# Optimization experiments

Measured on AMD Instinct MI355X. Metric: run time of the kernel, lower is better.

Reference implementation:

```python
import jax, jax.numpy as jnp
import numpy as np
import math

T, P, ITERS, H = 6, 8, 2, 8          # nr_types, num_proto, iters, n_head
D, F = 512, 1024                      # dim_proto, feature_dim (hidden_dim==D)
L = T * ITERS                         # 12 cross-attention layers


def _ln(x, g=None, b=None, eps=1e-5):
    m = x.mean(-1, keepdims=True)
    v = x.var(-1, keepdims=True)
    y = (x - m) * jax.lax.rsqrt(v + eps)
    if g is not None:
        y = y * g + b
    return y


def _forward(x_batch, batch_mask, node_type, pm_W, pm_b, pm_g, pm_bn,
             proto_logsigma, rand_mul, Wq, bq, Wk, bk, Wv, bv, Wo, bo,
             ag, ab, Wm1, bm1, lg, lb, Wm2, bm2, pg, pb):
    B, N, _ = x_batch.shape
    dt = x_batch.dtype
    bm = batch_mask.astype(dt)                                   # [B,N]
    onehot = jax.nn.one_hot(node_type, T, dtype=dt)              # [B,N,T]
    valid = bm * jnp.any(x_batch != 0, axis=-1).astype(dt)       # [B,N]
    mbt = onehot * valid[:, :, None]                             # [B,N,T]
    sums = jnp.einsum('bnt,bnf->btf', mbt, x_batch)              # per-(batch,type) sum
    cnt = mbt.sum(1)                                             # [B,T]
    fallback = x_batch.sum(1) / bm.sum(1, keepdims=True)         # [B,F]
    proto_mu = jnp.where(cnt[..., None] > 0,
                         sums / jnp.maximum(cnt, 1.0)[..., None],
                         fallback[:, None, :])                   # [B,T,F]

    # proto_mlp: Linear + LayerNorm + GELU (dropout = eval/identity)
    mu = jax.nn.gelu(_ln(proto_mu @ pm_W + pm_b, pm_g, pm_bn), approximate=False)  # [B,T,D]
    all_proto = mu[:, :, None, :] + jnp.exp(proto_logsigma)[None] * rand_mul[None]  # [B,T,P,D]

    dh = D // H
    scale = 1.0 / math.sqrt(dh)
    keymask = bm[:, None, None, :] == 0                          # [B,1,1,N]

    def layer(q, i):
        resid = q                                                 # [B,P,D]
        k = _ln((x_batch @ Wk[i] + bk[i]).reshape(B, N, H, dh))   # QK-LayerNorm (no affine)
        v = (x_batch @ Wv[i] + bv[i]).reshape(B, N, H, dh)
        qh = _ln((q @ Wq[i] + bq[i]).reshape(B, P, H, dh))
        dots = jnp.einsum('bkhd,bnhd->bkhn', qh, k) * scale       # [B,P,H,N]
        dots = jnp.where(keymask, -jnp.inf, dots)
        attn = jax.nn.softmax(dots, axis=-1)
        upd = jnp.einsum('bnhd,bkhn->bkhd', v, attn).reshape(B, P, D)
        upd = upd @ Wo[i] + bo[i]
        q = resid + _ln(upd, ag[i], ab[i])
        h = jax.nn.gelu(_ln(q @ Wm1[i] + bm1[i], lg[i], lb[i]), approximate=False)
        h = h @ Wm2[i] + bm2[i]
        return q + _ln(h, pg[i], pb[i])

    outs = []
    c = 0
    for i in range(T):
        p = all_proto[:, i]
        for _ in range(ITERS):
            p = layer(p, c)
            c += 1
        outs.append(p)
    prototypes = jnp.stack(outs, axis=1)                          # [B,T,P,D]
    return prototypes, proto_mu


def setup_inputs() -> dict:
    key = jax.random.key(0)
    ks = jax.random.split(key, 40)
    B, N = 4, 4096
    sc = 0.02

    def rn(i, shape, s=sc):
        return jax.random.normal(ks[i], shape, jnp.float32) * s

    inp = {
        'x_batch': jax.random.normal(ks[0], (B, N, F), jnp.float32),
        'batch_mask': jax.random.randint(ks[1], (B, N), 0, 2, jnp.int32),
        'node_type': jax.random.randint(ks[2], (B, N), 0, T, jnp.int32),
        'pm_W': rn(3, (F, D)), 'pm_b': jnp.zeros((D,)),
        'pm_g': jnp.ones((D,)), 'pm_bn': jnp.zeros((D,)),
        'proto_logsigma': rn(4, (T, 1, D), 0.05),
        'rand_mul': jax.random.normal(ks[5], (T, P, D), jnp.float32),
        'Wq': rn(6, (L, D, D)), 'bq': jnp.zeros((L, D)),
        'Wk': rn(7, (L, F, D)), 'bk': jnp.zeros((L, D)),
        'Wv': rn(8, (L, F, D)), 'bv': jnp.zeros((L, D)),
        'Wo': rn(9, (L, D, D)), 'bo': jnp.zeros((L, D)),
        'ag': jnp.ones((L, D)), 'ab': jnp.zeros((L, D)),
        'Wm1': rn(10, (L, D, D)), 'bm1': jnp.zeros((L, D)),
        'lg': jnp.ones((L, D)), 'lb': jnp.zeros((L, D)),
        'Wm2': rn(11, (L, D, D)), 'bm2': jnp.zeros((L, D)),
        'pg': jnp.ones((L, D)), 'pb': jnp.zeros((L, D)),
    }
    return inp


def reference(x_batch, batch_mask, node_type, pm_W, pm_b, pm_g, pm_bn,
              proto_logsigma, rand_mul, Wq, bq, Wk, bk, Wv, bv, Wo, bo,
              ag, ab, Wm1, bm1, lg, lb, Wm2, bm2, pg, pb):
    return _forward(x_batch, batch_mask, node_type, pm_W, pm_b, pm_g, pm_bn,
                    proto_logsigma, rand_mul, Wq, bq, Wk, bk, Wv, bv, Wo, bo,
                    ag, ab, Wm1, bm1, lg, lb, Wm2, bm2, pg, pb)
```

## Files before the change

### kernel.cpp

```cpp
#include <hip/hip_runtime.h>
#include <hip/hip_bf16.h>
#include <stdint.h>

#define TT 6
#define PP 8
#define HH 8
#define DD 512
#define FF 1024
#define DH 64
#define NB 4
#define NN 4096
#define LL 12
#define NCH 16
#define CHK 256

typedef __attribute__((ext_vector_type(8))) short short8v;
typedef __attribute__((ext_vector_type(4))) float f32x4;
typedef __attribute__((ext_vector_type(4))) unsigned short u16x4;
typedef __attribute__((ext_vector_type(8))) unsigned short u16x8;
typedef unsigned short u16;

__device__ __forceinline__ float bf2f(u16 u){
  union { unsigned int i; float f; } x; x.i = ((unsigned int)u) << 16; return x.f;
}
__device__ __forceinline__ u16 f2bf(float f){
  union { float f; unsigned int i; } x; x.f = f;
  unsigned int r = x.i + 0x7fffu + ((x.i >> 16) & 1u);
  return (u16)(r >> 16);
}
__device__ __forceinline__ float wave_sum(float x){
  #pragma unroll
  for (int o = 32; o > 0; o >>= 1) x += __shfl_xor(x, o);
  return x;
}
__device__ __forceinline__ float ldf(const void* p, size_t i, int f32){
  float v;
  if (f32) v = ((const float*)p)[i];
  else     v = bf2f(((const u16*)p)[i]);
  return v;
}
__device__ __forceinline__ float gemv_vec(const float* __restrict__ xs,
    const void* __restrict__ W, size_t wbase, int ktot, int wf32,
    float* __restrict__ red, int tid){
  int g = tid & 63, sl = tid >> 6;
  int kpw = ktot >> 3;
  float a[8] = {0,0,0,0,0,0,0,0};
  if (wf32){
    const float* Wp = (const float*)W + wbase + (size_t)(sl*kpw)*DD + g*8;
    #pragma unroll 4
    for (int i = 0; i < kpw; ++i){
      float xv = xs[sl*kpw + i];
      f32x4 lo = *(const f32x4*)(Wp + (size_t)i*DD);
      f32x4 hi = *(const f32x4*)(Wp + (size_t)i*DD + 4);
      a[0]+=xv*lo.x; a[1]+=xv*lo.y; a[2]+=xv*lo.z; a[3]+=xv*lo.w;
      a[4]+=xv*hi.x; a[5]+=xv*hi.y; a[6]+=xv*hi.z; a[7]+=xv*hi.w;
    }
  } else {
    const u16* Wp = (const u16*)W + wbase + (size_t)(sl*kpw)*DD + g*8;
    #pragma unroll 4
    for (int i = 0; i < kpw; ++i){
      float xv = xs[sl*kpw + i];
      u16x8 w8 = *(const u16x8*)(Wp + (size_t)i*DD);
      #pragma unroll
      for (int j = 0; j < 8; ++j) a[j] += xv * bf2f(w8[j]);
    }
  }
  #pragma unroll
  for (int j = 0; j < 8; ++j) red[sl*512 + g*8 + j] = a[j];
  __syncthreads();
  float y = 0;
  #pragma unroll
  for (int s2 = 0; s2 < 8; ++s2) y += red[s2*512 + tid];
  return y;
}
__device__ __forceinline__ void glds16(const void* g, void* l){
#if __has_builtin(__builtin_amdgcn_global_load_lds)
  __builtin_amdgcn_global_load_lds(
      (const __attribute__((address_space(1))) void*)g,
      (__attribute__((address_space(3))) void*)l, 16, 0, 0);
#else
  *(u16x8*)l = *(const u16x8*)g;
#endif
}
__device__ __forceinline__ void tail_gemm8(f32x4 acc[4], const u16* __restrict__ Bp,
    const u16* As, int l15, int q4, int n0w){
  #pragma unroll
  for (int ni = 0; ni < 4; ++ni){ f32x4 z = {0,0,0,0}; acc[ni] = z; }
  #pragma unroll 2
  for (int k0 = 0; k0 < 512; k0 += 32){
    short8v bf[4], af;
    #pragma unroll
    for (int ni = 0; ni < 4; ++ni)
      bf[ni] = *(const short8v*)(Bp + (size_t)(n0w + ni*16 + l15)*DD + k0 + q4*8);
    af = *(const short8v*)(As + l15*520 + k0 + q4*8);
    #pragma unroll
    for (int ni = 0; ni < 4; ++ni)
      acc[ni] = __builtin_amdgcn_mfma_f32_16x16x32_bf16(af, bf[ni], acc[ni], 0, 0, 0);
  }
}
__device__ __forceinline__ void row_ln8(const f32x4 acc[4],
    float* red1, float* red2, int w, int l15, int q4,
    float mv[4], float rv[4]){
  float s1[4], s2[4];
  #pragma unroll
  for (int r = 0; r < 4; ++r){
    float a0=acc[0][r], a1=acc[1][r], a2=acc[2][r], a3=acc[3][r];
    s1[r] = (a0+a1)+(a2+a3);
    s2[r] = (a0*a0+a1*a1)+(a2*a2+a3*a3);
  }
  #pragma unroll
  for (int o = 1; o < 16; o <<= 1)
    #pragma unroll
    for (int r = 0; r < 4; ++r){
      s1[r] += __shfl_xor(s1[r], o);
      s2[r] += __shfl_xor(s2[r], o);
    }
  if (l15 == 0){
    #pragma unroll
    for (int r = 0; r < 4; ++r){
      int row = q4*4 + r;
      red1[row*8 + w] = s1[r];
      red2[row*8 + w] = s2[r];
    }
  }
  __syncthreads();
  #pragma unroll
  for (int r = 0; r < 4; ++r){
    int row = q4*4 + r;
    float S1 = 0, S2 = 0;
    #pragma unroll
    for (int j = 0; j < 8; ++j){ S1 += red1[row*8+j]; S2 += red2[row*8+j]; }
    float m = S1 * (1.f/DD);
    float var = S2 * (1.f/DD) - m*m;
    mv[r] = m;
    rv[r] = rsqrtf(var + 1e-5f);
  }
  __syncthreads();
}

__global__ void k_detect(const void* __restrict__ X, int* __restrict__ flag){
  int tid = threadIdx.x;
  const u16* u = (const u16*)X;
  int bad = 0;
  for (int i = tid; i < 8192; i += 256){
    int ex = (u[i] >> 7) & 0xFF;
    if (ex >= 0x90) bad = 1;
  }
  __shared__ int s;
  if (tid == 0) s = 0;
  __syncthreads();
  if (bad) s = 1;
  __syncthreads();
  if (tid == 0) *flag = s;
}

__global__ void k_xbv(const void* __restrict__ X, u16* __restrict__ Xb,
                      const int* __restrict__ bm, float* __restrict__ valid,
                      const int* __restrict__ flagp){
  int f32 = *flagp;
  int bid = blockIdx.x, tid = threadIdx.x;
  size_t idx = (size_t)bid*FF + tid*4;
  bool a;
  if (f32){
    f32x4 v = *(const f32x4*)((const float*)X + idx);
    u16x4 o; o.x=f2bf(v.x); o.y=f2bf(v.y); o.z=f2bf(v.z); o.w=f2bf(v.w);
    *(u16x4*)(Xb+idx) = o;
    a = (v.x!=0.f)||(v.y!=0.f)||(v.z!=0.f)||(v.w!=0.f);
  } else {
    u16x4 v = *(const u16x4*)((const u16*)X + idx);
    *(u16x4*)(Xb+idx) = v;
    a = (bf2f(v.x)!=0.f)||(bf2f(v.y)!=0.f)||(bf2f(v.z)!=0.f)||(bf2f(v.w)!=0.f);
  }
  __shared__ int flag;
  if (tid==0) flag = 0;
  __syncthreads();
  if (a) flag = 1;
  __syncthreads();
  if (tid==0) valid[bid] = (flag && bm[bid]) ? 1.f : 0.f;
}

__global__ void k_compact(const int* __restrict__ bm, int* __restrict__ nidx,
                          int* __restrict__ cntc){
  int b = blockIdx.x, tid = threadIdx.x;
  __shared__ int csum[256];
  __shared__ int pref[257];
  int base = b*NN + tid*16;
  int f[16]; int loc = 0;
  #pragma unroll
  for (int i = 0; i < 16; ++i){ f[i] = (bm[base+i] != 0); loc += f[i]; }
  csum[tid] = loc;
  __syncthreads();
  if (tid == 0){
    pref[0] = 0;
    for (int j = 0; j < 256; ++j) pref[j+1] = pref[j] + csum[j];
  }
  __syncthreads();
  int off = b*NN + pref[tid];
  #pragma unroll
  for (int i = 0; i < 16; ++i){ if (f[i]) nidx[off++] = tid*16 + i; }
  if (tid == 0) cntc[b] = pref[256];
}

__global__ void k_wbfT(const void* __restrict__ Wq, const void* __restrict__ Wo,
                       const void* __restrict__ Wm1, const void* __restrict__ Wm2,
                       u16* __restrict__ Wt, const int* __restrict__ flagp){
  int f32 = *flagp;
  int z = blockIdx.z;
  int fam = z / LL;
  const void* src = (fam==0) ? Wq : (fam==1) ? Wo : (fam==2) ? Wm1 : Wm2;
  size_t sbase = (size_t)(z % LL) * DD * DD;
  __shared__ u16 tile[32][33];
  int d0 = blockIdx.x*32, k0 = blockIdx.y*32;
  int tx = threadIdx.x, ty = threadIdx.y;
  #pragma unroll
  for (int i = 0; i < 4; ++i){
    size_t idx = sbase + (size_t)(k0 + ty + i*8)*DD + d0 + tx;
    u16 v;
    if (f32) v = f2bf(((const float*)src)[idx]);
    else     v = ((const u16*)src)[idx];
    tile[ty + i*8][tx] = v;
  }
  __syncthreads();
  #pragma unroll
  for (int i = 0; i < 4; ++i)
    Wt[((size_t)z*DD + d0 + ty + i*8)*DD + k0 + tx] = tile[tx][ty + i*8];
}

__global__ void k_cnt(const float* __restrict__ valid, const int* __restrict__ bm,
                      const int* __restrict__ ntype, float* __restrict__ cnt,
                      float* __restrict__ bmsum){
  int b = blockIdx.x; int tid = threadIdx.x;
  float c[TT] = {0,0,0,0,0,0}; float cb = 0;
  for (int n = tid; n < NN; n += 256){
    float v = valid[b*NN + n];
    int ty = ntype[b*NN + n];
    #pragma unroll
    for (int t = 0; t < TT; ++t) c[t] += (ty==t) ? v : 0.f;
    cb += bm[b*NN+n] ? 1.f : 0.f;
  }
  __shared__ float sc_[TT+1];
  if (tid < TT+1) sc_[tid] = 0.f;
  __syncthreads();
  #pragma unroll
  for (int t = 0; t < TT; ++t) atomicAdd(&sc_[t], c[t]);
  atomicAdd(&sc_[TT], cb);
  __syncthreads();
  if (tid < TT) cnt[b*TT + tid] = sc_[tid];
  if (tid == TT) bmsum[b] = sc_[TT];
}

__global__ void k_colsum(const u16* __restrict__ Xb, const float* __restrict__ valid,
                         const int* __restrict__ ntype, float* __restrict__ colsums,
                         float* __restrict__ coltotal){
  int f0 = threadIdx.x * 4;
  int b = blockIdx.z;
  int n0 = blockIdx.y * 64;
  float acc[TT][4] = {};
  float tot[4] = {0,0,0,0};
  for (int i = 0; i < 64; ++i){
    int n = n0 + i;
    u16x4 xv4 = *(const u16x4*)(Xb + ((size_t)(b*NN+n))*FF + f0);
    float v = valid[b*NN+n];
    int ty = ntype[b*NN+n];
    #pragma unroll
    for (int j = 0; j < 4; ++j){
      float xv = bf2f(xv4[j]);
      tot[j] += xv;
      float xvv = xv * v;
      #pragma unroll
      for (int t = 0; t < TT; ++t) acc[t][j] += (ty==t) ? xvv : 0.f;
    }
  }
  #pragma unroll
  for (int t = 0; t < TT; ++t)
    #pragma unroll
    for (int j = 0; j < 4; ++j)
      atomicAdd(&colsums[((size_t)(b*TT+t))*FF + f0 + j], acc[t][j]);
  #pragma unroll
  for (int j = 0; j < 4; ++j)
    atomicAdd(&coltotal[b*FF + f0 + j], tot[j]);
}

__global__ void k_protomu(const float* __restrict__ colsums, const float* __restrict__ coltotal,
                          const float* __restrict__ cnt, const float* __restrict__ bmsum,
                          float* __restrict__ proto_mu, void* __restrict__ dout,
                          const int* __restrict__ flagp){
  int f32 = *flagp;
  const size_t OFFP = (size_t)NB*TT*PP*DD;
  int bt = blockIdx.x; int b = bt / TT;
  int tid = threadIdx.x;
  float cv = cnt[bt];
  float inv = 1.f / fmaxf(cv, 1.f);
  float fbinv = 1.f / bmsum[b];
  for (int f = tid; f < FF; f += 256){
    float pm = (cv > 0.f) ? colsums[(size_t)bt*FF + f] * inv
                          : coltotal[b*FF + f] * fbinv;
    proto_mu[(size_t)bt*FF + f] = pm;
    if (f32) ((float*)dout)[OFFP + (size_t)bt*FF + f] = pm;
    else     ((u16*)dout)[OFFP + (size_t)bt*FF + f] = f2bf(pm);
  }
}

__global__ void __launch_bounds__(512) k_mu(const float* __restrict__ proto_mu,
   const void* __restrict__ pmW, const void* __restrict__ pmb,
   const void* __restrict__ pmg, const void* __restrict__ pmbn,
   const void* __restrict__ lsig, const void* __restrict__ rmul,
   float* __restrict__ qstate, const int* __restrict__ flagp){
  int f32 = *flagp;
  int bt = blockIdx.x; int b = bt/TT, t = bt%TT;
  int d = threadIdx.x;
  __shared__ float xs[FF];
  __shared__ float red[4096];
  __shared__ float r1[8], r2[8];
  xs[d] = proto_mu[(size_t)bt*FF + d];
  xs[d+512] = proto_mu[(size_t)bt*FF + d + 512];
  __syncthreads();
  float acc = ldf(pmb, d, f32) + gemv_vec(xs, pmW, 0, FF, f32, red, d);
  int lane = d & 63, wid = d >> 6;
  float s1 = wave_sum(acc), s2 = wave_sum(acc*acc);
  if (lane==0){ r1[wid]=s1; r2[wid]=s2; }
  __syncthreads();
  float m=0, qq=0;
  #pragma unroll
  for (int i=0;i<8;++i){ m+=r1[i]; qq+=r2[i]; }
  m *= (1.f/DD); float var = qq*(1.f/DD) - m*m;
  float y = (acc - m) * rsqrtf(var + 1e-5f) * ldf(pmg, d, f32) + ldf(pmbn, d, f32);
  float mu = 0.5f * y * (1.f + erff(y * 0.70710678118654752f));
  #pragma unroll
  for (int p = 0; p < PP; ++p){
    float rv = ldf(rmul, (size_t)(t*PP+p)*DD + d, f32);
    float ls = ldf(lsig, (size_t)t*DD + d, f32);
    qstate[(((size_t)(b*TT+t))*PP + p)*DD + d] = mu + expf(ls) * rv;
  }
}

__global__ void k_transpose(const void* __restrict__ Wk, const void* __restrict__ Wv,
                            u16* __restrict__ TK, u16* __restrict__ TV,
                            int tlo, int s, const int* __restrict__ flagp){
  int f32 = *flagp;
  int ti = blockIdx.z >> 1, kv = blockIdx.z & 1;
  int c = 2*(tlo+ti)+s;
  size_t eoff = (size_t)c*FF*DD;
  const void* W = kv ? Wv : Wk;
  u16* T = (kv ? TV : TK) + (size_t)ti*FF*DD;
  __shared__ u16 tile[32][33];
  int n0 = blockIdx.x * 32, k0 = blockIdx.y * 32;
  int tx = threadIdx.x, ty = threadIdx.y;
  #pragma unroll
  for (int i = 0; i < 4; ++i){
    size_t idx = eoff + (size_t)(k0 + ty + i*8)*DD + n0 + tx;
    u16 v;
    if (f32) v = f2bf(((const float*)W)[idx]);
    else     v = ((const u16*)W)[idx];
    tile[ty + i*8][tx] = v;
  }
  __syncthreads();
  #pragma unroll
  for (int i = 0; i < 4; ++i)
    T[(size_t)(n0 + ty + i*8)*FF + k0 + tx] = tile[tx][ty + i*8];
}

__global__ void __launch_bounds__(512) k_kvgemm(const u16* __restrict__ Xb,
    const u16* __restrict__ TK, const u16* __restrict__ TV,
    const void* __restrict__ bk, const void* __restrict__ bv,
    u16* __restrict__ Kb, u16* __restrict__ Vb,
    const int* __restrict__ nidx, const int* __restrict__ cntc,
    int tlo, int s, int nt, const int* __restrict__ flagp){
  int f32 = *flagp;
  int orig = blockIdx.x;
  int x = orig & 7, r = orig >> 3;
  int bx = r / nt, pr = r - bx*nt;
  int pairg = x*nt + pr;
  int by = pairg & 3; int kvti = pairg >> 2; int kv = kvti & 1; int ti = kvti >> 1;
  int b = bx >> 4, jt = bx & 15;
  int cnt = cntc[b];
  if (jt*256 >= cnt) return;
  int c = 2*(tlo+ti)+s;
  size_t boff = (size_t)c*DD;
  const u16* WT = (kv ? TV : TK) + (size_t)ti*FF*DD;
  const void* bias = kv ? bv : bk;
  u16* out = (kv ? Vb : Kb) + (size_t)ti*((size_t)NB*NN*DD);
  int n0 = by*128;
  __shared__ __align__(16) char LDS[3*24576];
  int tid = threadIdx.x, wid = tid >> 6, lane = tid & 63;
  int wr = wid >> 1, wcn = wid & 1;
  const u16* gp0; const u16* gp1; const u16* gp2;
  int lo0, lo1, lo2;
  {
    const u16* gps[3]; int los[3];
    #pragma unroll
    for (int i = 0; i < 3; ++i){
      int e = tid + i*512;
      if (e < 1024){
        int row = e>>2, sp = e&3;
        int ssrc = sp ^ (((row>>3)&1)<<1);
        int cl = jt*256 + row; if (cl >= cnt) cl = cnt-1;
        int grow = nidx[b*NN + cl];
        gps[i] = Xb + ((size_t)b*NN + grow)*FF + ssrc*8;
        los[i] = e*16;
      } else {
        int e2 = e - 1024;
        int row = e2>>2, sp = e2&3;
        int ssrc = sp ^ (((row>>3)&1)<<1);
        gps[i] = WT + (size_t)(n0 + row)*FF + ssrc*8;
        los[i] = 16384 + e2*16;
      }
    }
    gp0=gps[0]; gp1=gps[1]; gp2=gps[2];
    lo0=los[0]; lo1=los[1]; lo2=los[2];
  }
#define STAGE(T) { char* bb_ = LDS + ((T)%3)*24576; \
  glds16(gp0 + (T)*32, bb_ + lo0); glds16(gp1 + (T)*32, bb_ + lo1); \
  glds16(gp2 + (T)*32, bb_ + lo2); }
  int ke = (lane>>4) ^ (((lane>>3)&1)<<1);
  int arow[4], brow[4];
  #pragma unroll
  for (int mi = 0; mi < 4; ++mi)
    arow[mi] = (wr*64 + mi*16 + (lane&15))*64 + ke*16;
  #pragma unroll
  for (int ni = 0; ni < 4; ++ni)
    brow[ni] = 16384 + (wcn*64 + ni*16 + (lane&15))*64 + ke*16;
  f32x4 acc[4][4] = {};
  STAGE(0);
  STAGE(1);
  asm volatile("s_waitcnt vmcnt(3)" ::: "memory");
  __builtin_amdgcn_sched_barrier(0);
  __builtin_amdgcn_s_barrier();
  __builtin_amdgcn_sched_barrier(0);
  #pragma unroll
  for (int t = 0; t < 32; ++t){
    const char* Bbuf = LDS + (t%3)*24576;
    short8v af[4], bf[4];
    #pragma unroll
    for (int mi = 0; mi < 4; ++mi)
      af[mi] = *(const short8v*)(Bbuf + arow[mi]);
    #pragma unroll
    for (int ni = 0; ni < 4; ++ni)
      bf[ni] = *(const short8v*)(Bbuf + brow[ni]);
    if (t + 2 <= 31) STAGE(t+2);
    __builtin_amdgcn_s_setprio(1);
    #pragma unroll
    for (int mi = 0; mi < 4; ++mi)
      #pragma unroll
      for (int ni = 0; ni < 4; ++ni)
        acc[mi][ni] = __builtin_amdgcn_mfma_f32_16x16x32_bf16(af[mi], bf[ni], acc[mi][ni], 0, 0, 0);
    __builtin_amdgcn_s_setprio(0);
    if (t < 30)       asm volatile("s_waitcnt vmcnt(3)" ::: "memory");
    else if (t == 30) asm volatile("s_waitcnt vmcnt(0)" ::: "memory");
    __builtin_amdgcn_sched_barrier(0);
    if (t < 31){
      __builtin_amdgcn_s_barrier();
      __builtin_amdgcn_sched_barrier(0);
    }
  }
#undef STAGE
  #pragma unroll
  for (int mi = 0; mi < 4; ++mi){
    #pragma unroll
    for (int ni = 0; ni < 4; ++ni){
      int col = n0 + wcn*64 + ni*16 + (lane & 15);
      int h = col >> 6, dh = col & 63;
      float bvf = ldf(bias, boff + col, f32);
      #pragma unroll
      for (int r2 = 0; r2 < 4; ++r2){
        int row = jt*256 + wr*64 + mi*16 + (lane>>4)*4 + r2;
        out[(((size_t)(b*HH + h))*NN + row)*DH + dh] = f2bf(acc[mi][ni][r2] + bvf);
      }
    }
  }
}

__global__ void __launch_bounds__(512) k_qproj(const float* __restrict__ qstate,
      const void* __restrict__ Wq, const void* __restrict__ bq,
      float* __restrict__ qh, int tlo, int s, int wmode,
      const int* __restrict__ flagp){
  int f32 = *flagp;
  int wf32 = wmode ? f32 : 0;
  int z = blockIdx.x; int ti = z >> 5, rr = z & 31;
  int b = rr >> 3, p = rr & 7;
  int t = tlo + ti, c = 2*t + s;
  size_t woff = (size_t)c*DD*DD, boff = (size_t)c*DD;
  int d = threadIdx.x;
  __shared__ float xs[DD];
  __shared__ float red[4096];
  const float* xrow = qstate + (((size_t)(b*TT+t))*PP + p)*DD;
  xs[d] = xrow[d];
  __syncthreads();
  float acc = ldf(bq, boff + d, f32) + gemv_vec(xs, Wq, woff, DD, wf32, red, d);
  float s1 = wave_sum(acc) * (1.f/DH);
  float s2 = wave_sum(acc*acc) * (1.f/DH);
  float var = s2 - s1*s1;
  qh[(size_t)z*DD + d] = (acc - s1) * rsqrtf(var + 1e-5f);
}

__global__ void __launch_bounds__(512) k_attnA(const u16* __restrict__ Kb,
     const u16* __restrict__ Vb, const float* __restrict__ qh,
     const int* __restrict__ cntc, float* __restrict__ Opart, float* __restrict__ lpart){
  int ic = blockIdx.x, bh = blockIdx.y, ti = blockIdx.z;
  int b = bh >> 3, h = bh & 7;
  int cnt = cntc[b];
  if (ic*CHK >= cnt) return;
  int tid = threadIdx.x, p8 = tid >> 6, ln = tid & 63;
  int r8 = ln >> 3, g = ln & 7;
  __shared__ __align__(16) char KV[65536];
  __shared__ float qs[PP*DH];
  __shared__ float qsum[PP];
  __shared__ float e_lds[CHK*9];
  int rem = cnt - ic*CHK;
  float qv = qh[((size_t)(ti*32 + b*PP + p8))*DD + h*DH + ln];
  size_t tioff = (size_t)ti*((size_t)NB*NN*DD);
  const u16* Kbase = Kb + tioff + ((size_t)(b*HH + h)*NN + (size_t)ic*CHK)*DH;
  const u16* Vbase = Vb + tioff + ((size_t)(b*HH + h)*NN + (size_t)ic*CHK)*DH;
  #pragma unroll
  for (int i = 0; i < 4; ++i){
    int e = tid + i*512;
    int row = e >> 3, sp = e & 7;
    int rr = row < rem ? row : rem-1;
    glds16(Kbase + (size_t)rr*DH + sp*8, (char*)KV + e*16);
  }
  #pragma unroll
  for (int i = 0; i < 4; ++i){
    int e = tid + i*512;
    int row = e >> 3, sp = e & 7;
    int ss = sp ^ (row & 7);
    int rr = row < rem ? row : rem-1;
    glds16(Vbase + (size_t)rr*DH + ss*8, (char*)KV + 32768 + e*16);
  }
  qs[p8*DH + ln] = qv;
  {
    float sQ = wave_sum(qv);
    if (ln == 0) qsum[p8] = sQ;
  }
  asm volatile("s_waitcnt vmcnt(4) lgkmcnt(0)" ::: "memory");
  __builtin_amdgcn_sched_barrier(0);
  __builtin_amdgcn_s_barrier();
  __builtin_amdgcn_sched_barrier(0);
  #pragma unroll
  for (int it = 0; it < CHK/64; ++it){
    int nl = it*64 + p8*8 + r8;
    u16x8 kv8 = *(const u16x8*)((const char*)KV + nl*128 + g*16);
    float kf[8];
    #pragma unroll
    for (int e = 0; e < 8; ++e) kf[e] = bf2f(kv8[e]);
    float sm = 0, sq = 0;
    #pragma unroll
    for (int e = 0; e < 8; ++e){ sm += kf[e]; sq += kf[e]*kf[e]; }
    #pragma unroll
    for (int o = 1; o < 8; o <<= 1){
      sm += __shfl_xor(sm, o);
      sq += __shfl_xor(sq, o);
    }
    sm *= (1.f/DH); sq = sq*(1.f/DH) - sm*sm;
    float inv = rsqrtf(sq + 1e-5f);
    float ap[8];
    #pragma unroll
    for (int p = 0; p < 8; ++p){
      f32x4 qa = *(const f32x4*)&qs[p*DH + g*8];
      f32x4 qb = *(const f32x4*)&qs[p*DH + g*8 + 4];
      ap[p] = kf[0]*qa.x + kf[1]*qa.y + kf[2]*qa.z + kf[3]*qa.w
            + kf[4]*qb.x + kf[5]*qb.y + kf[6]*qb.z + kf[7]*qb.w;
    }
    #pragma unroll
    for (int o = 1; o < 8; o <<= 1){
      #pragma unroll
      for (int p = 0; p < 8; ++p) ap[p] += __shfl_xor(ap[p], o);
    }
    float dg = (g==0)?ap[0]:(g==1)?ap[1]:(g==2)?ap[2]:(g==3)?ap[3]
             : (g==4)?ap[4]:(g==5)?ap[5]:(g==6)?ap[6]:ap[7];
    float sv = (dg - sm*qsum[g]) * inv * 0.125f;
    e_lds[nl*9 + g] = (nl < rem) ? __expf(sv) : 0.f;
  }
  __syncthreads();
  {
    float lp = 0;
    #pragma unroll
    for (int j = 0; j < CHK/64; ++j) lp += e_lds[(ln + j*64)*9 + p8];
    lp = wave_sum(lp);
    if (ln == 0) lpart[((size_t)(ti*32+bh)*NCH + ic)*PP + p8] = lp;
  }
  {
    float a0=0,a1=0,a2=0,a3=0,a4=0,a5=0,a6=0,a7=0;
    int vseg = (r8 ^ g) * 16;
    #pragma unroll 4
    for (int m = 0; m < CHK/8; ++m){
      float e = e_lds[(g + m*8)*9 + p8];
      u16x8 vv = *(const u16x8*)((const char*)KV + 32768 + (g + m*8)*128 + vseg);
      a0 += e*bf2f(vv[0]); a1 += e*bf2f(vv[1]);
      a2 += e*bf2f(vv[2]); a3 += e*bf2f(vv[3]);
      a4 += e*bf2f(vv[4]); a5 += e*bf2f(vv[5]);
      a6 += e*bf2f(vv[6]); a7 += e*bf2f(vv[7]);
    }
    #pragma unroll
    for (int o = 1; o < 8; o <<= 1){
      a0 += __shfl_xor(a0, o); a1 += __shfl_xor(a1, o);
      a2 += __shfl_xor(a2, o); a3 += __shfl_xor(a3, o);
      a4 += __shfl_xor(a4, o); a5 += __shfl_xor(a5, o);
      a6 += __shfl_xor(a6, o); a7 += __shfl_xor(a7, o);
    }
    if (g == 0){
      float* op = Opart + ((size_t)(ti*32+bh)*NCH + ic)*512 + p8*64 + r8*8;
      f32x4 lo = {a0,a1,a2,a3}, hi = {a4,a5,a6,a7};
      *(f32x4*)op = lo;
      *((f32x4*)op + 1) = hi;
    }
  }
}

__global__ void __launch_bounds__(512) k_tailm(
    const float* __restrict__ Opart, const float* __restrict__ lpart,
    const int* __restrict__ cntc,
    float* __restrict__ qstate, float* __restrict__ qh,
    const u16* __restrict__ Wt,
    const void* __restrict__ bo, const void* __restrict__ ag, const void* __restrict__ ab,
    const void* __restrict__ bm1, const void* __restrict__ lg, const void* __restrict__ lb,
    const void* __restrict__ bm2, const void* __restrict__ pg, const void* __restrict__ pb,
    const void* __restrict__ bq,
    int tlo, int s, int nt, const int* __restrict__ flagp){
  int f32 = *flagp;
  int ti = blockIdx.x & 7, b = blockIdx.x >> 3;
  if (ti >= nt) return;
  int t = tlo + ti, c = 2*t + s;
  int tid = threadIdx.x;
  int w = tid >> 6, lane = tid & 63, q4 = lane >> 4, l15 = lane & 15;
  int n0w = w*64;
  size_t boff = (size_t)c*DD;
  const size_t famSz = (size_t)LL*DD*DD;
  __shared__ u16 As[16*520];
  __shared__ float red1[128], red2[128];
  __shared__ float lval[64];
  int nch = (cntc[b] + CHK - 1) / CHK;
  for (int i = tid; i < 16*520; i += 512) As[i] = 0;
  if (tid < 64){
    int p = tid >> 3, hh = tid & 7;
    float l = 0;
    for (int ic = 0; ic < nch; ++ic)
      l += lpart[((size_t)(ti*32 + b*8 + hh)*NCH + ic)*PP + p];
    lval[tid] = 1.f / l;
  }
  __syncthreads();
  {
    int hh = tid >> 6, dd = tid & 63;
    #pragma unroll
    for (int p = 0; p < 8; ++p){
      float o = 0;
      for (int ic = 0; ic < nch; ++ic)
        o += Opart[((size_t)(ti*32 + b*8 + hh)*NCH + ic)*512 + p*64 + dd];
      As[p*520 + hh*64 + dd] = f2bf(o * lval[p*8 + hh]);
    }
  }
  __syncthreads();
  f32x4 acc[4], q2[4];
  float mv[4], rv[4];
  size_t qoffb = ((size_t)(b*TT+t))*PP*DD;
  {
    const u16* Bp = Wt + famSz + (size_t)c*DD*DD;
    tail_gemm8(acc, Bp, As, l15, q4, n0w);
    #pragma unroll
    for (int ni = 0; ni < 4; ++ni){
      float bv = ldf(bo, boff + n0w + ni*16 + l15, f32);
      #pragma unroll
      for (int r = 0; r < 4; ++r) acc[ni][r] += bv;
    }
    row_ln8(acc, red1, red2, w, l15, q4, mv, rv);
    #pragma unroll
    for (int ni = 0; ni < 4; ++ni){
      int col = n0w + ni*16 + l15;
      float gm = ldf(ag, boff + col, f32), bt = ldf(ab, boff + col, f32);
      #pragma unroll
      for (int r = 0; r < 4; ++r){
        int row = q4*4 + r;
        float y = (acc[ni][r] - mv[r])*rv[r]*gm + bt;
        float res = (q4 < 2) ? qstate[qoffb + (size_t)row*DD + col] : 0.f;
        q2[ni][r] = res + y;
      }
    }
    if (q4 < 2){
      #pragma unroll
      for (int r = 0; r < 4; ++r){
        int row = q4*4 + r;
        #pragma unroll
        for (int ni = 0; ni < 4; ++ni)
          As[row*520 + n0w + ni*16 + l15] = f2bf(q2[ni][r]);
      }
    }
  }
  __syncthreads();
  {
    const u16* Bp = Wt + 2*famSz + (size_t)c*DD*DD;
    tail_gemm8(acc, Bp, As, l15, q4, n0w);
    #pragma unroll
    for (int ni = 0; ni < 4; ++ni){
      float bv = ldf(bm1, boff + n0w + ni*16 + l15, f32);
      #pragma unroll
      for (int r = 0; r < 4; ++r) acc[ni][r] += bv;
    }
    row_ln8(acc, red1, red2, w, l15, q4, mv, rv);
    #pragma unroll
    for (int ni = 0; ni < 4; ++ni){
      int col = n0w + ni*16 + l15;
      float gm = ldf(lg, boff + col, f32), bt = ldf(lb, boff + col, f32);
      #pragma unroll
      for (int r = 0; r < 4; ++r){
        int row = q4*4 + r;
        float y = (acc[ni][r] - mv[r])*rv[r]*gm + bt;
        y = 0.5f*y*(1.f + erff(y*0.70710678118654752f));
        if (q4 < 2) As[row*520 + col] = f2bf(y);
      }
    }
  }
  __syncthreads();
  {
    const u16* Bp = Wt + 3*famSz + (size_t)c*DD*DD;
    tail_gemm8(acc, Bp, As, l15, q4, n0w);
    #pragma unroll
    for (int ni = 0; ni < 4; ++ni){
      float bv = ldf(bm2, boff + n0w + ni*16 + l15, f32);
      #pragma unroll
      for (int r = 0; r < 4; ++r) acc[ni][r] += bv;
    }
    row_ln8(acc, red1, red2, w, l15, q4, mv, rv);
    #pragma unroll
    for (int ni = 0; ni < 4; ++ni){
      int col = n0w + ni*16 + l15;
      float gm = ldf(pg, boff + col, f32), bt = ldf(pb, boff + col, f32);
      #pragma unroll
      for (int r = 0; r < 4; ++r){
        int row = q4*4 + r;
        float outv = q2[ni][r] + (acc[ni][r] - mv[r])*rv[r]*gm + bt;
        if (q4 < 2){
          qstate[qoffb + (size_t)row*DD + col] = outv;
          if (s == 0) As[row*520 + col] = f2bf(outv);
        }
      }
    }
  }
  if (s == 0){
    __syncthreads();
    const u16* Bp = Wt + (size_t)(c+1)*DD*DD;
    tail_gemm8(acc, Bp, As, l15, q4, n0w);
    #pragma unroll
    for (int ni = 0; ni < 4; ++ni){
      float bv = ldf(bq, (size_t)(c+1)*DD + n0w + ni*16 + l15, f32);
      #pragma unroll
      for (int r = 0; r < 4; ++r) acc[ni][r] += bv;
    }
    float s1[4], s2[4];
    #pragma unroll
    for (int r = 0; r < 4; ++r){
      float a0=acc[0][r], a1=acc[1][r], a2=acc[2][r], a3=acc[3][r];
      s1[r] = (a0+a1)+(a2+a3);
      s2[r] = (a0*a0+a1*a1)+(a2*a2+a3*a3);
    }
    #pragma unroll
    for (int o = 1; o < 16; o <<= 1)
      #pragma unroll
      for (int r = 0; r < 4; ++r){
        s1[r] += __shfl_xor(s1[r], o);
        s2[r] += __shfl_xor(s2[r], o);
      }
    if (q4 < 2){
      #pragma unroll
      for (int r = 0; r < 4; ++r){
        int row = q4*4 + r;
        float m = s1[r] * (1.f/DH);
        float var = s2[r] * (1.f/DH) - m*m;
        float ri = rsqrtf(var + 1e-5f);
        #pragma unroll
        for (int ni = 0; ni < 4; ++ni){
          int col = n0w + ni*16 + l15;
          qh[((size_t)(ti*32 + b*8 + row))*DD + col] = (acc[ni][r] - m)*ri;
        }
      }
    }
  }
}

__global__ void __launch_bounds__(512) k_tail(
    const float* __restrict__ Opart, const float* __restrict__ lpart,
    const int* __restrict__ cntc,
    float* __restrict__ qstate, float* __restrict__ qh,
    const void* __restrict__ Wo_, const void* __restrict__ Wm1_,
    const void* __restrict__ Wm2_, const void* __restrict__ Wq_,
    const void* __restrict__ bo, const void* __restrict__ ag, const void* __restrict__ ab,
    const void* __restrict__ bm1, const void* __restrict__ lg, const void* __restrict__ lb,
    const void* __restrict__ bm2, const void* __restrict__ pg, const void* __restrict__ pb,
    const void* __restrict__ bq,
    int tlo, int s, int wmode, const int* __restrict__ flagp){
  int f32 = *flagp;
  int wf32 = wmode ? f32 : 0;
  int z = blockIdx.x; int ti = z >> 5, rr = z & 31;
  int b = rr >> 3, p = rr & 7;
  int t = tlo + ti, c = 2*t + s;
  int d = threadIdx.x;
  int h = d >> 6, dd = d & 63;
  int lane = d & 63, wid = d >> 6;
  size_t qoff = (((size_t)(b*TT+t))*PP + p)*DD;
  size_t boff = (size_t)c*DD;
  size_t w0 = (size_t)c*DD*DD;
  __shared__ float xs[DD];
  __shared__ float red[4096];
  __shared__ float r1[8], r2[8];
  int nch = (cntc[b] + CHK - 1) / CHK;
  float o = 0, l = 0;
  for (int ic = 0; ic < nch; ++ic){
    o += Opart[((size_t)(ti*32 + b*8 + h)*NCH + ic)*512 + p*64 + dd];
    l += lpart[((size_t)(ti*32 + b*8 + h)*NCH + ic)*PP + p];
  }
  float upd = o / l;
  xs[d] = upd;
  __syncthreads();
  float acc = ldf(bo, boff + d, f32) + gemv_vec(xs, Wo_, w0, DD, wf32, red, d);
  {
    float s1 = wave_sum(acc), s2 = wave_sum(acc*acc);
    if (lane == 0){ r1[wid] = s1; r2[wid] = s2; }
  }
  __syncthreads();
  float m = 0, qv = 0;
  #pragma unroll
  for (int i = 0; i < 8; ++i){ m += r1[i]; qv += r2[i]; }
  m *= (1.f/DD); float var = qv*(1.f/DD) - m*m;
  float y = (acc - m)*rsqrtf(var + 1e-5f)*ldf(ag, boff+d, f32) + ldf(ab, boff+d, f32);
  float q2 = qstate[qoff + d] + y;
  __syncthreads();
  xs[d] = q2;
  __syncthreads();
  float acc2 = ldf(bm1, boff + d, f32) + gemv_vec(xs, Wm1_, w0, DD, wf32, red, d);
  {
    float s1 = wave_sum(acc2), s2 = wave_sum(acc2*acc2);
    if (lane == 0){ r1[wid] = s1; r2[wid] = s2; }
  }
  __syncthreads();
  m = 0; qv = 0;
  #pragma unroll
  for (int i = 0; i < 8; ++i){ m += r1[i]; qv += r2[i]; }
  m *= (1.f/DD); var = qv*(1.f/DD) - m*m;
  float y2 = (acc2 - m)*rsqrtf(var + 1e-5f)*ldf(lg, boff+d, f32) + ldf(lb, boff+d, f32);
  y2 = 0.5f*y2*(1.f + erff(y2*0.70710678118654752f));
  __syncthreads();
  xs[d] = y2;
  __syncthreads();
  float acc3 = ldf(bm2, boff + d, f32) + gemv_vec(xs, Wm2_, w0, DD, wf32, red, d);
  {
    float s1 = wave_sum(acc3), s2 = wave_sum(acc3*acc3);
    if (lane == 0){ r1[wid] = s1; r2[wid] = s2; }
  }
  __syncthreads();
  m = 0; qv = 0;
  #pragma unroll
  for (int i = 0; i < 8; ++i){ m += r1[i]; qv += r2[i]; }
  m *= (1.f/DD); var = qv*(1.f/DD) - m*m;
  float y3 = (acc3 - m)*rsqrtf(var + 1e-5f)*ldf(pg, boff+d, f32) + ldf(pb, boff+d, f32);
  float outv = q2 + y3;
  qstate[qoff + d] = outv;
  if (s == 0){
    __syncthreads();
    xs[d] = outv;
    __syncthreads();
    size_t w1 = (size_t)(c+1)*DD*DD;
    float accq = ldf(bq, (size_t)(c+1)*DD + d, f32) + gemv_vec(xs, Wq_, w1, DD, wf32, red, d);
    float t1 = wave_sum(accq) * (1.f/DH);
    float t2 = wave_sum(accq*accq) * (1.f/DH);
    float var2 = t2 - t1*t1;
    qh[(size_t)z*DD + d] = (accq - t1) * rsqrtf(var2 + 1e-5f);
  }
}

__global__ void k_out(const float* __restrict__ qstate, void* __restrict__ dout,
                      const int* __restrict__ flagp){
  int f32 = *flagp;
  int i = blockIdx.x*256 + threadIdx.x;
  if (f32) ((float*)dout)[i] = qstate[i];
  else     ((u16*)dout)[i] = f2bf(qstate[i]);
}

extern "C" void kernel_launch(void* const* d_in, const int* in_sizes, int n_in,
                              void* d_out, int out_size, void* d_ws, size_t ws_size,
                              hipStream_t stream){
  (void)in_sizes; (void)n_in; (void)out_size;
  const void* X   = d_in[0];
  const int* bm    = (const int*)d_in[1];
  const int* ntype = (const int*)d_in[2];
  const void* pmW = d_in[3];  const void* pmb = d_in[4];
  const void* pmg = d_in[5];  const void* pmbn= d_in[6];
  const void* lsig= d_in[7];  const void* rmul= d_in[8];
  const void* Wq  = d_in[9];  const void* bq  = d_in[10];
  const void* Wk  = d_in[11]; const void* bk  = d_in[12];
  const void* Wv  = d_in[13]; const void* bv  = d_in[14];
  const void* Wo  = d_in[15]; const void* bo  = d_in[16];
  const void* ag  = d_in[17]; const void* ab  = d_in[18];
  const void* Wm1 = d_in[19]; const void* bm1 = d_in[20];
  const void* lg  = d_in[21]; const void* lb  = d_in[22];
  const void* Wm2 = d_in[23]; const void* bm2 = d_in[24];
  const void* pg  = d_in[25]; const void* pb  = d_in[26];

  char* ws = (char*)d_ws;
  int*   flagp    = (int*)(ws + 0);
  float* cnt      = (float*)(ws + 256);
  float* bmsum    = (float*)(ws + 512);
  float* colsums  = (float*)(ws + 768);
  float* coltotal = (float*)(ws + 99072);
  float* valid    = (float*)(ws + 115456);
  float* proto_mu = (float*)(ws + 180992);
  float* qstate   = (float*)(ws + 279296);
  int*   cntc     = (int*)(ws + 672512);
  int*   nidx     = (int*)(ws + 672768);

  size_t off = 738304;
  auto take = [&](size_t bytes)->char*{
    char* p = ws + off; off = (off + bytes + 255) & ~(size_t)255; return p;
  };
  u16* Xbf = (u16*)take((size_t)NB*NN*FF*2);

  const size_t perT = (size_t)65536
                    + 16384
                    + 1048576
                    + 2*1048576
                    + 2*16777216;
  size_t base = off;
  int nt = 1;
  if      (ws_size >= base + 6*perT + 65536) nt = 6;
  else if (ws_size >= base + 3*perT + 65536) nt = 3;
  else if (ws_size >= base + 2*perT + 65536) nt = 2;

  float* qh    = (float*)take((size_t)nt*65536);
  float* lpart = (float*)take((size_t)nt*16384);
  float* Opart = (float*)take((size_t)nt*1048576);
  u16*   WkT   = (u16*)take((size_t)nt*1048576);
  u16*   WvT   = (u16*)take((size_t)nt*1048576);
  u16*   Kb    = (u16*)take((size_t)nt*16777216);
  u16*   Vb    = (u16*)take((size_t)nt*16777216);

  const size_t wtBytes = (size_t)4*LL*DD*DD*2;
  int useWt = (ws_size >= off + wtBytes + 65536) ? 1 : 0;
  u16* Wt = useWt ? (u16*)take(wtBytes) : nullptr;

  hipMemsetAsync(ws + 256, 0, 115200, stream);
  k_detect<<<1, 256, 0, stream>>>(X, flagp);
  k_xbv<<<NB*NN, 256, 0, stream>>>(X, Xbf, bm, valid, flagp);
  k_compact<<<NB, 256, 0, stream>>>(bm, nidx, cntc);
  if (useWt)
    k_wbfT<<<dim3(16, 16, 4*LL), dim3(32, 8), 0, stream>>>(Wq, Wo, Wm1, Wm2, Wt, flagp);
  k_cnt<<<NB, 256, 0, stream>>>(valid, bm, ntype, cnt, bmsum);
  k_colsum<<<dim3(1, 64, NB), 256, 0, stream>>>(Xbf, valid, ntype, colsums, coltotal);
  k_protomu<<<NB*TT, 256, 0, stream>>>(colsums, coltotal, cnt, bmsum, proto_mu, d_out, flagp);
  k_mu<<<NB*TT, 512, 0, stream>>>(proto_mu, pmW, pmb, pmg, pmbn, lsig, rmul, qstate, flagp);

  for (int tlo = 0; tlo < TT; tlo += nt){
    for (int s = 0; s < 2; ++s){
      k_transpose<<<dim3(16, 32, 2*nt), dim3(32, 8), 0, stream>>>(
          Wk, Wv, WkT, WvT, tlo, s, flagp);
      k_kvgemm<<<64*8*nt, 512, 0, stream>>>(
          Xbf, WkT, WvT, bk, bv, Kb, Vb, nidx, cntc, tlo, s, nt, flagp);
      if (s == 0)
        k_qproj<<<nt*32, 512, 0, stream>>>(qstate, Wq, bq, qh, tlo, s, 1, flagp);
      k_attnA<<<dim3(NCH, 32, nt), 512, 0, stream>>>(Kb, Vb, qh, cntc, Opart, lpart);
      if (useWt)
        k_tailm<<<32, 512, 0, stream>>>(Opart, lpart, cntc, qstate, qh, Wt,
            bo, ag, ab, bm1, lg, lb, bm2, pg, pb, bq, tlo, s, nt, flagp);
      else
        k_tail<<<nt*32, 512, 0, stream>>>(Opart, lpart, cntc, qstate, qh,
            Wo, Wm1, Wm2, Wq, bo, ag, ab, bm1, lg, lb, bm2, pg, pb, bq,
            tlo, s, 1, flagp);
    }
  }
  k_out<<<NB*TT*PP*DD/256, 256, 0, stream>>>(qstate, d_out, flagp);
}
```

Measured before the change: 694.7 us.

## Fuse X conversion with type column sums and counts; prestage bf16 weights

Merges the X bf16 conversion, validity detection, per-type counts and column sums into one kernel that reads X once. The separate valid buffer and the count, colsum and protomu kernels go away. proto_mu computation moves into k_mu. pm_W and Wq are pre-converted to bf16 so the GEMV and q-projection read half the bytes. The final tail layer writes the output directly, which skips k_out. The trade-off is more atomics on cnt/bmsum and extra conversion launches for the weights.

```diff
diff --git a/kernel.cpp b/kernel.cpp
--- a/kernel.cpp
+++ b/kernel.cpp
@@ -154,29 +154,81 @@
   if (tid == 0) *flag = s;
 }
 
-__global__ void k_xbv(const void* __restrict__ X, u16* __restrict__ Xb,
-                      const int* __restrict__ bm, float* __restrict__ valid,
+__global__ void k_cvt(const void* __restrict__ src, u16* __restrict__ dst,
                       const int* __restrict__ flagp){
   int f32 = *flagp;
-  int bid = blockIdx.x, tid = threadIdx.x;
-  size_t idx = (size_t)bid*FF + tid*4;
-  bool a;
+  size_t i = ((size_t)blockIdx.x*256 + threadIdx.x)*4;
   if (f32){
-    f32x4 v = *(const f32x4*)((const float*)X + idx);
+    f32x4 v = *(const f32x4*)((const float*)src + i);
     u16x4 o; o.x=f2bf(v.x); o.y=f2bf(v.y); o.z=f2bf(v.z); o.w=f2bf(v.w);
-    *(u16x4*)(Xb+idx) = o;
-    a = (v.x!=0.f)||(v.y!=0.f)||(v.z!=0.f)||(v.w!=0.f);
+    *(u16x4*)(dst+i) = o;
   } else {
-    u16x4 v = *(const u16x4*)((const u16*)X + idx);
-    *(u16x4*)(Xb+idx) = v;
-    a = (bf2f(v.x)!=0.f)||(bf2f(v.y)!=0.f)||(bf2f(v.z)!=0.f)||(bf2f(v.w)!=0.f);
-  }
-  __shared__ int flag;
-  if (tid==0) flag = 0;
-  __syncthreads();
-  if (a) flag = 1;
-  __syncthreads();
-  if (tid==0) valid[bid] = (flag && bm[bid]) ? 1.f : 0.f;
+    *(u16x4*)(dst+i) = *(const u16x4*)((const u16*)src + i);
+  }
+}
+
+__global__ void k_xcv(const void* __restrict__ X, u16* __restrict__ Xb,
+                      const int* __restrict__ bm, const int* __restrict__ ntype,
+                      float* __restrict__ colsums, float* __restrict__ coltotal,
+                      float* __restrict__ cnt, float* __restrict__ bmsum,
+                      const int* __restrict__ flagp){
+  int f32 = *flagp;
+  int b = blockIdx.y, n0 = blockIdx.x * 64;
+  int tid = threadIdx.x;
+  int f0 = tid * 4;
+  __shared__ int sflag[64];
+  __shared__ float scnt[TT+1];
+  if (tid < 64) sflag[tid] = 0;
+  if (tid < TT+1) scnt[tid] = 0.f;
+  __syncthreads();
+  float acc[TT][4] = {};
+  float tot[4] = {0,0,0,0};
+  for (int i = 0; i < 64; ++i){
+    int n = n0 + i;
+    size_t idx = (size_t)(b*NN+n)*FF + f0;
+    u16x4 xb;
+    bool a;
+    if (f32){
+      f32x4 v = *(const f32x4*)((const float*)X + idx);
+      xb.x=f2bf(v.x); xb.y=f2bf(v.y); xb.z=f2bf(v.z); xb.w=f2bf(v.w);
+      a = (v.x!=0.f)||(v.y!=0.f)||(v.z!=0.f)||(v.w!=0.f);
+    } else {
+      xb = *(const u16x4*)((const u16*)X + idx);
+      a = (bf2f(xb.x)!=0.f)||(bf2f(xb.y)!=0.f)||(bf2f(xb.z)!=0.f)||(bf2f(xb.w)!=0.f);
+    }
+    *(u16x4*)(Xb+idx) = xb;
+    if (a) sflag[i] = 1;
+    float vbm = (bm[b*NN+n] != 0) ? 1.f : 0.f;
+    int ty = ntype[b*NN+n];
+    #pragma unroll
+    for (int j = 0; j < 4; ++j){
+      float xv = bf2f(xb[j]);
+      tot[j] += xv;
+      float xvv = xv * vbm;
+      #pragma unroll
+      for (int t = 0; t < TT; ++t) acc[t][j] += (ty==t) ? xvv : 0.f;
+    }
+  }
+  __syncthreads();
+  if (tid < 64){
+    int n = n0 + tid;
+    int bmv = (bm[b*NN+n] != 0);
+    if (bmv){
+      if (sflag[tid]) atomicAdd(&scnt[ntype[b*NN+n]], 1.f);
+      atomicAdd(&scnt[TT], 1.f);
+    }
+  }
+  #pragma unroll
+  for (int t = 0; t < TT; ++t)
+    #pragma unroll
+    for (int j = 0; j < 4; ++j)
+      atomicAdd(&colsums[((size_t)(b*TT+t))*FF + f0 + j], acc[t][j]);
+  #pragma unroll
+  for (int j = 0; j < 4; ++j)
+    atomicAdd(&coltotal[b*FF + f0 + j], tot[j]);
+  __syncthreads();
+  if (tid < TT) atomicAdd(&cnt[b*TT + tid], scnt[tid]);
+  if (tid == TT) atomicAdd(&bmsum[b], scnt[TT]);
 }
 
 __global__ void k_compact(const int* __restrict__ bm, int* __restrict__ nidx,
@@ -226,96 +278,36 @@
     Wt[((size_t)z*DD + d0 + ty + i*8)*DD + k0 + tx] = tile[tx][ty + i*8];
 }
 
-__global__ void k_cnt(const float* __restrict__ valid, const int* __restrict__ bm,
-                      const int* __restrict__ ntype, float* __restrict__ cnt,
-                      float* __restrict__ bmsum){
-  int b = blockIdx.x; int tid = threadIdx.x;
-  float c[TT] = {0,0,0,0,0,0}; float cb = 0;
-  for (int n = tid; n < NN; n += 256){
-    float v = valid[b*NN + n];
-    int ty = ntype[b*NN + n];
-    #pragma unroll
-    for (int t = 0; t < TT; ++t) c[t] += (ty==t) ? v : 0.f;
-    cb += bm[b*NN+n] ? 1.f : 0.f;
-  }
-  __shared__ float sc_[TT+1];
-  if (tid < TT+1) sc_[tid] = 0.f;
-  __syncthreads();
-  #pragma unroll
-  for (int t = 0; t < TT; ++t) atomicAdd(&sc_[t], c[t]);
-  atomicAdd(&sc_[TT], cb);
-  __syncthreads();
-  if (tid < TT) cnt[b*TT + tid] = sc_[tid];
-  if (tid == TT) bmsum[b] = sc_[TT];
-}
-
-__global__ void k_colsum(const u16* __restrict__ Xb, const float* __restrict__ valid,
-                         const int* __restrict__ ntype, float* __restrict__ colsums,
-                         float* __restrict__ coltotal){
-  int f0 = threadIdx.x * 4;
-  int b = blockIdx.z;
-  int n0 = blockIdx.y * 64;
-  float acc[TT][4] = {};
-  float tot[4] = {0,0,0,0};
-  for (int i = 0; i < 64; ++i){
-    int n = n0 + i;
-    u16x4 xv4 = *(const u16x4*)(Xb + ((size_t)(b*NN+n))*FF + f0);
-    float v = valid[b*NN+n];
-    int ty = ntype[b*NN+n];
-    #pragma unroll
-    for (int j = 0; j < 4; ++j){
-      float xv = bf2f(xv4[j]);
-      tot[j] += xv;
-      float xvv = xv * v;
-      #pragma unroll
-      for (int t = 0; t < TT; ++t) acc[t][j] += (ty==t) ? xvv : 0.f;
-    }
-  }
-  #pragma unroll
-  for (int t = 0; t < TT; ++t)
-    #pragma unroll
-    for (int j = 0; j < 4; ++j)
-      atomicAdd(&colsums[((size_t)(b*TT+t))*FF + f0 + j], acc[t][j]);
-  #pragma unroll
-  for (int j = 0; j < 4; ++j)
-    atomicAdd(&coltotal[b*FF + f0 + j], tot[j]);
-}
-
-__global__ void k_protomu(const float* __restrict__ colsums, const float* __restrict__ coltotal,
-                          const float* __restrict__ cnt, const float* __restrict__ bmsum,
-                          float* __restrict__ proto_mu, void* __restrict__ dout,
-                          const int* __restrict__ flagp){
-  int f32 = *flagp;
-  const size_t OFFP = (size_t)NB*TT*PP*DD;
-  int bt = blockIdx.x; int b = bt / TT;
-  int tid = threadIdx.x;
-  float cv = cnt[bt];
-  float inv = 1.f / fmaxf(cv, 1.f);
-  float fbinv = 1.f / bmsum[b];
-  for (int f = tid; f < FF; f += 256){
-    float pm = (cv > 0.f) ? colsums[(size_t)bt*FF + f] * inv
-                          : coltotal[b*FF + f] * fbinv;
-    proto_mu[(size_t)bt*FF + f] = pm;
-    if (f32) ((float*)dout)[OFFP + (size_t)bt*FF + f] = pm;
-    else     ((u16*)dout)[OFFP + (size_t)bt*FF + f] = f2bf(pm);
-  }
-}
-
-__global__ void __launch_bounds__(512) k_mu(const float* __restrict__ proto_mu,
-   const void* __restrict__ pmW, const void* __restrict__ pmb,
+__global__ void __launch_bounds__(512) k_mu(const float* __restrict__ colsums,
+   const float* __restrict__ coltotal, const float* __restrict__ cnt,
+   const float* __restrict__ bmsum,
+   const void* __restrict__ pmWx, const void* __restrict__ pmb,
    const void* __restrict__ pmg, const void* __restrict__ pmbn,
    const void* __restrict__ lsig, const void* __restrict__ rmul,
-   float* __restrict__ qstate, const int* __restrict__ flagp){
+   float* __restrict__ qstate, void* __restrict__ dout, int wmode,
+   const int* __restrict__ flagp){
   int f32 = *flagp;
+  int wf32 = wmode ? f32 : 0;
+  const size_t OFFP = (size_t)NB*TT*PP*DD;
   int bt = blockIdx.x; int b = bt/TT, t = bt%TT;
   int d = threadIdx.x;
   __shared__ float xs[FF];
   __shared__ float red[4096];
   __shared__ float r1[8], r2[8];
-  xs[d] = proto_mu[(size_t)bt*FF + d];
-  xs[d+512] = proto_mu[(size_t)bt*FF + d + 512];
-  __syncthreads();
-  float acc = ldf(pmb, d, f32) + gemv_vec(xs, pmW, 0, FF, f32, red, d);
+  float cv = cnt[bt];
+  float inv = 1.f / fmaxf(cv, 1.f);
+  float fbinv = 1.f / bmsum[b];
+  #pragma unroll
+  for (int h = 0; h < 2; ++h){
+    int f = d + h*512;
+    float pm = (cv > 0.f) ? colsums[(size_t)bt*FF + f] * inv
+                          : coltotal[b*FF + f] * fbinv;
+    xs[f] = pm;
+    if (f32) ((float*)dout)[OFFP + (size_t)bt*FF + f] = pm;
+    else     ((u16*)dout)[OFFP + (size_t)bt*FF + f] = f2bf(pm);
+  }
+  __syncthreads();
+  float acc = ldf(pmb, d, f32) + gemv_vec(xs, pmWx, 0, FF, wf32, red, d);
   int lane = d & 63, wid = d >> 6;
   float s1 = wave_sum(acc), s2 = wave_sum(acc*acc);
   if (lane==0){ r1[wid]=s1; r2[wid]=s2; }
@@ -614,7 +606,7 @@
     const void* __restrict__ bo, const void* __restrict__ ag, const void* __restrict__ ab,
     const void* __restrict__ bm1, const void* __restrict__ lg, const void* __restrict__ lb,
     const void* __restrict__ bm2, const void* __restrict__ pg, const void* __restrict__ pb,
-    const void* __restrict__ bq,
+    const void* __restrict__ bq, void* __restrict__ dout,
     int tlo, int s, int nt, const int* __restrict__ flagp){
   int f32 = *flagp;
   int ti = blockIdx.x & 7, b = blockIdx.x >> 3;
@@ -730,6 +722,10 @@
         if (q4 < 2){
           qstate[qoffb + (size_t)row*DD + col] = outv;
           if (s == 0) As[row*520 + col] = f2bf(outv);
+          else {
+            if (f32) ((float*)dout)[qoffb + (size_t)row*DD + col] = outv;
+            else     ((u16*)dout)[qoffb + (size_t)row*DD + col] = f2bf(outv);
+          }
         }
       }
     }
@@ -899,8 +895,6 @@
   float* bmsum    = (float*)(ws + 512);
   float* colsums  = (float*)(ws + 768);
   float* coltotal = (float*)(ws + 99072);
-  float* valid    = (float*)(ws + 115456);
-  float* proto_mu = (float*)(ws + 180992);
   float* qstate   = (float*)(ws + 279296);
   int*   cntc     = (int*)(ws + 672512);
   int*   nidx     = (int*)(ws + 672768);
@@ -934,16 +928,29 @@
   int useWt = (ws_size >= off + wtBytes + 65536) ? 1 : 0;
   u16* Wt = useWt ? (u16*)take(wtBytes) : nullptr;
 
+  const size_t pmwbB = (size_t)FF*DD*2;
+  const size_t wqbB  = (size_t)LL*DD*DD*2;
+  int useCvt = (ws_size >= off + pmwbB + wqbB + 65536) ? 1 : 0;
+  u16* pmWb = useCvt ? (u16*)take(pmwbB) : nullptr;
+  u16* Wqb  = useCvt ? (u16*)take(wqbB)  : nullptr;
+
   hipMemsetAsync(ws + 256, 0, 115200, stream);
   k_detect<<<1, 256, 0, stream>>>(X, flagp);
-  k_xbv<<<NB*NN, 256, 0, stream>>>(X, Xbf, bm, valid, flagp);
   k_compact<<<NB, 256, 0, stream>>>(bm, nidx, cntc);
   if (useWt)
     k_wbfT<<<dim3(16, 16, 4*LL), dim3(32, 8), 0, stream>>>(Wq, Wo, Wm1, Wm2, Wt, flagp);
-  k_cnt<<<NB, 256, 0, stream>>>(valid, bm, ntype, cnt, bmsum);
-  k_colsum<<<dim3(1, 64, NB), 256, 0, stream>>>(Xbf, valid, ntype, colsums, coltotal);
-  k_protomu<<<NB*TT, 256, 0, stream>>>(colsums, coltotal, cnt, bmsum, proto_mu, d_out, flagp);
-  k_mu<<<NB*TT, 512, 0, stream>>>(proto_mu, pmW, pmb, pmg, pmbn, lsig, rmul, qstate, flagp);
+  if (useCvt){
+    k_cvt<<<(FF*DD)/1024, 256, 0, stream>>>(pmW, pmWb, flagp);
+    k_cvt<<<(LL*DD*DD)/1024, 256, 0, stream>>>(Wq, Wqb, flagp);
+  }
+  k_xcv<<<dim3(64, NB), 256, 0, stream>>>(X, Xbf, bm, ntype, colsums, coltotal,
+                                          cnt, bmsum, flagp);
+  if (useCvt)
+    k_mu<<<NB*TT, 512, 0, stream>>>(colsums, coltotal, cnt, bmsum,
+        pmWb, pmb, pmg, pmbn, lsig, rmul, qstate, d_out, 0, flagp);
+  else
+    k_mu<<<NB*TT, 512, 0, stream>>>(colsums, coltotal, cnt, bmsum,
+        pmW, pmb, pmg, pmbn, lsig, rmul, qstate, d_out, 1, flagp);
 
   for (int tlo = 0; tlo < TT; tlo += nt){
     for (int s = 0; s < 2; ++s){
@@ -951,17 +958,22 @@
           Wk, Wv, WkT, WvT, tlo, s, flagp);
       k_kvgemm<<<64*8*nt, 512, 0, stream>>>(
           Xbf, WkT, WvT, bk, bv, Kb, Vb, nidx, cntc, tlo, s, nt, flagp);
-      if (s == 0)
-        k_qproj<<<nt*32, 512, 0, stream>>>(qstate, Wq, bq, qh, tlo, s, 1, flagp);
+      if (s == 0){
+        if (useCvt)
+          k_qproj<<<nt*32, 512, 0, stream>>>(qstate, Wqb, bq, qh, tlo, s, 0, flagp);
+        else
+          k_qproj<<<nt*32, 512, 0, stream>>>(qstate, Wq, bq, qh, tlo, s, 1, flagp);
+      }
       k_attnA<<<dim3(NCH, 32, nt), 512, 0, stream>>>(Kb, Vb, qh, cntc, Opart, lpart);
       if (useWt)
         k_tailm<<<32, 512, 0, stream>>>(Opart, lpart, cntc, qstate, qh, Wt,
-            bo, ag, ab, bm1, lg, lb, bm2, pg, pb, bq, tlo, s, nt, flagp);
+            bo, ag, ab, bm1, lg, lb, bm2, pg, pb, bq, d_out, tlo, s, nt, flagp);
       else
         k_tail<<<nt*32, 512, 0, stream>>>(Opart, lpart, cntc, qstate, qh,
             Wo, Wm1, Wm2, Wq, bo, ag, ab, bm1, lg, lb, bm2, pg, pb, bq,
             tlo, s, 1, flagp);
     }
   }
-  k_out<<<NB*TT*PP*DD/256, 256, 0, stream>>>(qstate, d_out, flagp);
-}
+  if (!useWt)
+    k_out<<<NB*TT*PP*DD/256, 256, 0, stream>>>(qstate, d_out, flagp);
+}
```

After: 664.9 us. 4.3% less time.
